# Performance work log

Measured on AMD Instinct MI355X. Metric: run time of the kernel, lower is better.

The kernel has to match this reference:

```python
import jax, jax.numpy as jnp
import numpy as np

N_NODES = 100000


def _gcn_conv(x, W, b, src, dst, n):
    # PyG GCNConv (default): add self-loops, norm = deg^{-1/2}[src] * deg^{-1/2}[dst]
    # degree computed on target nodes (col) with unit edge weights, then
    # out[i] = sum_{(j->i)} norm_ji * (x_j @ W) + b
    loops = jnp.arange(n, dtype=src.dtype)
    s = jnp.concatenate([src, loops])
    d = jnp.concatenate([dst, loops])
    deg = jax.ops.segment_sum(jnp.ones_like(d, dtype=x.dtype), d, num_segments=n)
    dinv = jnp.where(deg > 0, jax.lax.rsqrt(deg), 0.0)
    h = x @ W                                  # [n, out_dim]
    norm = (dinv[s] * dinv[d])[:, None]        # [E+n, 1]
    msg = h[s] * norm                          # gather + scale
    out = jax.ops.segment_sum(msg, d, num_segments=n)  # scatter-add to targets
    return out + b


def setup_inputs() -> dict:
    key = jax.random.key(0)
    ks = jax.random.split(key, 4)
    x = jax.random.normal(ks[0], (N_NODES, 128), dtype=jnp.float32)
    edge_index = jax.random.randint(ks[1], (2, 1600000), 0, N_NODES, dtype=jnp.int64)
    W1 = jax.random.normal(ks[2], (128, 16), dtype=jnp.float32) * (1.0 / np.sqrt(128))
    b1 = jnp.zeros((16,), dtype=jnp.float32)
    W2 = jax.random.normal(ks[3], (16, 3), dtype=jnp.float32) * (1.0 / np.sqrt(16))
    b2 = jnp.zeros((3,), dtype=jnp.float32)
    return {"x": x, "edge_index": edge_index, "W1": W1, "b1": b1, "W2": W2, "b2": b2}


def reference(x, edge_index, W1, b1, W2, b2):
    src, dst = edge_index[0], edge_index[1]
    n = x.shape[0]
    h = _gcn_conv(x, W1, b1, src, dst, n)
    h = jax.nn.relu(h)
    # F.dropout in eval mode == identity (deterministic baseline)
    h = _gcn_conv(h, W2, b2, src, dst, n)
    return jax.nn.log_softmax(h, axis=1)
```

## Files before the change

### kernel.cpp

```cpp
#include <hip/hip_runtime.h>
#include <hip/hip_fp16.h>
#include <math.h>


#define BSH 9
#define BNODES 512
#define P1 512
#define GROWS 64
#define K2BUF 10240

struct alignas(8) Half4 { __half x, y, z, w; };

__global__ void k1a_count(const int* __restrict__ dst, int* __restrict__ hist_t,
                          int NBK, int E) {
    __shared__ int lh[256];
    int t = threadIdx.x;
    lh[t] = 0;
    __syncthreads();
    int slice = (E + P1 - 1) / P1;
    int e0 = blockIdx.x * slice, e1 = min(E, e0 + slice);
    for (int e = e0 + t; e < e1; e += 256)
        atomicAdd(&lh[dst[e] >> BSH], 1);
    __syncthreads();
    for (int i = t; i < NBK; i += 256)
        hist_t[(size_t)i * P1 + blockIdx.x] = lh[i];
}

__global__ void kscan1(const int* __restrict__ hist_t, int* __restrict__ colpre_t,
                       int* __restrict__ btot, int NBK) {
    __shared__ int v[P1], part[256];
    int kb = blockIdx.x, t = threadIdx.x;
    v[t] = hist_t[(size_t)kb * P1 + t];
    v[t + 256] = hist_t[(size_t)kb * P1 + t + 256];
    __syncthreads();
    int a = v[2 * t], c = v[2 * t + 1];
    part[t] = a + c;
    __syncthreads();
    for (int o = 1; o < 256; o <<= 1) {
        int add = (t >= o) ? part[t - o] : 0;
        __syncthreads();
        part[t] += add;
        __syncthreads();
    }
    int pre = (t == 0) ? 0 : part[t - 1];
    colpre_t[(size_t)kb * P1 + 2 * t] = pre;
    colpre_t[(size_t)kb * P1 + 2 * t + 1] = pre + a;
    if (t == 255) btot[kb] = part[255];
}

__global__ void kscan2(const int* __restrict__ btot, int* __restrict__ bucket_base, int NBK) {
    __shared__ int s[256];
    int t = threadIdx.x;
    int orig = (t < NBK) ? btot[t] : 0;
    s[t] = orig;
    __syncthreads();
    for (int o = 1; o < 256; o <<= 1) {
        int add = (t >= o) ? s[t - o] : 0;
        __syncthreads();
        s[t] += add;
        __syncthreads();
    }
    if (t < NBK) {
        bucket_base[t] = s[t] - orig;
        if (t == NBK - 1) bucket_base[NBK] = s[t];
    }
}

__global__ void k1b_fat(const int* __restrict__ src, const int* __restrict__ dst,
                        const int* __restrict__ colpre_t, const int* __restrict__ bucket_base,
                        unsigned int* __restrict__ staging,
                        const float* __restrict__ x, const float* __restrict__ W1,
                        Half4* __restrict__ g1h, int NBK, int n, int E) {
    __shared__ float sx[GROWS * 132];
    __shared__ float4 sW4[512];
    int b = blockIdx.x;
    if (b < P1) {
        int* hist  = (int*)sx;
        int* cs    = hist + 256;
        int* loff  = hist + 512;
        int* cur   = hist + 768;
        int* buf   = hist + 1024;
        int* gaddr = buf + 3200;
        int t = threadIdx.x;
        hist[t] = 0; cur[t] = 0;
        for (int i = t; i < NBK; i += 256)
            loff[i] = bucket_base[i] + colpre_t[(size_t)i * P1 + b];
        __syncthreads();
        int slice = (E + P1 - 1) / P1;
        int e0 = b * slice, e1 = min(E, e0 + slice);
        int len = e1 - e0;
        for (int e = e0 + t; e < e1; e += 256)
            atomicAdd(&hist[dst[e] >> BSH], 1);
        __syncthreads();
        int h = hist[t];
        cs[t] = h;
        __syncthreads();
        for (int o = 1; o < 256; o <<= 1) {
            int add = (t >= o) ? cs[t - o] : 0;
            __syncthreads();
            cs[t] += add;
            __syncthreads();
        }
        int incl = cs[t];
        __syncthreads();
        cs[t] = incl - h;
        __syncthreads();
        for (int e = e0 + t; e < e1; e += 256) {
            int d = dst[e], s = src[e];
            int k = d >> BSH;
            int tk = atomicAdd(&cur[k], 1);
            int pos = cs[k] + tk;
            buf[pos] = (s << BSH) | (d & (BNODES - 1));
            gaddr[pos] = loff[k] + tk;
        }
        __syncthreads();
        for (int p = t; p < len; p += 256)
            staging[gaddr[p]] = (unsigned int)buf[p];
    } else {
        int t = threadIdx.x;
        int base = (b - P1) * GROWS;
        for (int i = t; i < 512; i += 256) sW4[i] = ((const float4*)W1)[i];
        for (int i = t; i < GROWS * 32; i += 256) {
            int r = i >> 5, c = i & 31;
            int row = base + r;
            float4 v = (row < n) ? ((const float4*)x)[(size_t)row * 32 + c]
                                 : make_float4(0.f, 0.f, 0.f, 0.f);
            *((float4*)&sx[r * 132 + c * 4]) = v;
        }
        __syncthreads();
        int r = t >> 2, c4 = t & 3;
        int row = base + r;
        if (row >= n) return;
        float4 acc = make_float4(0.f, 0.f, 0.f, 0.f);
        #pragma unroll 8
        for (int q = 0; q < 32; ++q) {
            float4 xv = *((const float4*)&sx[r * 132 + q * 4]);
            #pragma unroll
            for (int j = 0; j < 4; ++j) {
                float s = (j == 0) ? xv.x : (j == 1) ? xv.y : (j == 2) ? xv.z : xv.w;
                float4 w = sW4[(q * 4 + j) * 4 + c4];
                acc.x += s * w.x; acc.y += s * w.y; acc.z += s * w.z; acc.w += s * w.w;
            }
        }
        Half4 hh;
        hh.x = __float2half(acc.x); hh.y = __float2half(acc.y);
        hh.z = __float2half(acc.z); hh.w = __float2half(acc.w);
        g1h[(size_t)row * 4 + c4] = hh;
    }
}

__global__ void __launch_bounds__(1024) k2_bucket(
        const unsigned int* __restrict__ staging, const int* __restrict__ bucket_base,
        int* __restrict__ csr, int* __restrict__ deg, float* __restrict__ dinv,
        int* __restrict__ row_start, Half4* __restrict__ g1h, int n) {
    __shared__ int lh[BNODES], sc[BNODES], lcur[BNODES];
    __shared__ float ldv[BNODES];
    __shared__ int buf[K2BUF];
    int kb = blockIdx.x, t = threadIdx.x;
    int node0 = kb << BSH;
    int nloc = min(BNODES, n - node0);
    int ebase = bucket_base[kb], ecnt = bucket_base[kb + 1] - ebase;
    if (t < BNODES) { lh[t] = 0; lcur[t] = 0; }
    __syncthreads();
    for (int e = t; e < ecnt; e += 1024)
        atomicAdd(&lh[staging[ebase + e] & (BNODES - 1)], 1);
    __syncthreads();
    int own = 0;
    if (t < BNODES) { own = lh[t]; sc[t] = own; }
    __syncthreads();
    for (int o = 1; o < BNODES; o <<= 1) {
        int add = 0;
        if (t < BNODES && t >= o) add = sc[t - o];
        __syncthreads();
        if (t < BNODES) sc[t] += add;
        __syncthreads();
    }
    if (t < BNODES) {
        int excl = sc[t] - own;
        if (t < nloc) {
            deg[node0 + t] = own;
            row_start[node0 + t] = ebase + excl;
            float dv = rsqrtf((float)(own + 1));
            dinv[node0 + t] = dv;
            ldv[t] = dv;
        }
        sc[t] = excl;
    }
    __syncthreads();
    if (ecnt <= K2BUF) {
        for (int e = t; e < ecnt; e += 1024) {
            unsigned int p = staging[ebase + e];
            int loc = p & (BNODES - 1);
            int tk = atomicAdd(&lcur[loc], 1);
            buf[sc[loc] + tk] = (int)(p >> BSH);
        }
        __syncthreads();
        for (int p = t; p < ecnt; p += 1024)
            csr[ebase + p] = buf[p];
    } else {
        for (int e = t; e < ecnt; e += 1024) {
            unsigned int p = staging[ebase + e];
            int loc = p & (BNODES - 1);
            int tk = atomicAdd(&lcur[loc], 1);
            csr[ebase + sc[loc] + tk] = (int)(p >> BSH);
        }
    }
    for (int j = t; j < nloc * 4; j += 1024) {
        float dv = ldv[j >> 2];
        Half4 v = g1h[(size_t)node0 * 4 + j];
        v.x = __float2half(__half2float(v.x) * dv);
        v.y = __float2half(__half2float(v.y) * dv);
        v.z = __float2half(__half2float(v.z) * dv);
        v.w = __float2half(__half2float(v.w) * dv);
        g1h[(size_t)node0 * 4 + j] = v;
    }
}

__global__ void k_gather1(const uint4* __restrict__ g1q, const int* __restrict__ csr,
                          const int* __restrict__ row_start, const int* __restrict__ deg,
                          const float* __restrict__ dinv, const float* __restrict__ b1,
                          const float* __restrict__ W2, Half4* __restrict__ g2h, int n) {
    int idx = blockIdx.x * 256 + threadIdx.x;
    int i = idx >> 4, l = idx & 15;
    if (i >= n) return;
    int off = row_start[i], dg = deg[i];
    float acc[16];
    #pragma unroll
    for (int j = 0; j < 16; ++j) acc[j] = 0.f;
    if (l == 0) {
        uint4 p0 = g1q[2 * (size_t)i], p1 = g1q[2 * (size_t)i + 1];
        const __half2* h0 = reinterpret_cast<const __half2*>(&p0);
        const __half2* h1 = reinterpret_cast<const __half2*>(&p1);
        #pragma unroll
        for (int j = 0; j < 4; ++j) {
            float2 f0 = __half22float2(h0[j]);
            float2 f1 = __half22float2(h1[j]);
            acc[2 * j] += f0.x; acc[2 * j + 1] += f0.y;
            acc[8 + 2 * j] += f1.x; acc[9 + 2 * j] += f1.y;
        }
    }
    for (int k = l; k < dg; k += 16) {
        int s = csr[off + k];
        uint4 p0 = g1q[2 * (size_t)s], p1 = g1q[2 * (size_t)s + 1];
        const __half2* h0 = reinterpret_cast<const __half2*>(&p0);
        const __half2* h1 = reinterpret_cast<const __half2*>(&p1);
        #pragma unroll
        for (int j = 0; j < 4; ++j) {
            float2 f0 = __half22float2(h0[j]);
            float2 f1 = __half22float2(h1[j]);
            acc[2 * j] += f0.x; acc[2 * j + 1] += f0.y;
            acc[8 + 2 * j] += f1.x; acc[9 + 2 * j] += f1.y;
        }
    }
    #pragma unroll
    for (int m = 1; m < 16; m <<= 1) {
        #pragma unroll
        for (int j = 0; j < 16; ++j) acc[j] += __shfl_xor(acc[j], m);
    }
    if (l != 0) return;
    float di = dinv[i];
    float o0 = 0.f, o1 = 0.f, o2 = 0.f;
    #pragma unroll
    for (int c = 0; c < 16; ++c) {
        float z = fmaxf(0.f, di * acc[c] + b1[c]);
        o0 += z * W2[c * 3 + 0];
        o1 += z * W2[c * 3 + 1];
        o2 += z * W2[c * 3 + 2];
    }
    Half4 g;
    g.x = __float2half(di * o0); g.y = __float2half(di * o1);
    g.z = __float2half(di * o2); g.w = __float2half(0.f);
    g2h[i] = g;
}

__global__ void k_gather2(const Half4* __restrict__ g2h, const int* __restrict__ csr,
                          const int* __restrict__ row_start, const int* __restrict__ deg,
                          const float* __restrict__ dinv, const float* __restrict__ b2,
                          float* __restrict__ out, int n) {
    int idx = blockIdx.x * 256 + threadIdx.x;
    int i = idx >> 4, l = idx & 15;
    if (i >= n) return;
    int off = row_start[i], dg = deg[i];
    float v0 = 0.f, v1 = 0.f, v2 = 0.f;
    if (l == 0) {
        Half4 s = g2h[i];
        v0 = __half2float(s.x); v1 = __half2float(s.y); v2 = __half2float(s.z);
    }
    for (int e = l; e < dg; e += 16) {
        int s = csr[off + e];
        Half4 g = g2h[s];
        v0 += __half2float(g.x); v1 += __half2float(g.y); v2 += __half2float(g.z);
    }
    #pragma unroll
    for (int o = 1; o < 16; o <<= 1) {
        v0 += __shfl_xor(v0, o);
        v1 += __shfl_xor(v1, o);
        v2 += __shfl_xor(v2, o);
    }
    if (l >= 3) return;
    float di = dinv[i];
    float a0 = di * v0 + b2[0];
    float a1 = di * v1 + b2[1];
    float a2 = di * v2 + b2[2];
    float m = fmaxf(a0, fmaxf(a1, a2));
    float lse = logf(expf(a0 - m) + expf(a1 - m) + expf(a2 - m));
    float r = (l == 0) ? a0 : (l == 1) ? a1 : a2;
    out[(size_t)i * 3 + l] = r - m - lse;
}

extern "C" void kernel_launch(void* const* d_in, const int* in_sizes, int n_in,
                              void* d_out, int out_size, void* d_ws, size_t ws_size,
                              hipStream_t stream) {
    const float* x  = (const float*)d_in[0];
    const int*   ei = (const int*)d_in[1];
    const float* W1 = (const float*)d_in[2];
    const float* b1 = (const float*)d_in[3];
    const float* W2 = (const float*)d_in[4];
    const float* b2 = (const float*)d_in[5];
    float* out = (float*)d_out;

    const int n = in_sizes[0] / 128;
    const int E = in_sizes[1] / 2;
    const int* src = ei;
    const int* dst = ei + E;

    const int NBK = (n + BNODES - 1) >> BSH;

    auto align = [](size_t v) { return (v + 255) & ~(size_t)255; };
    char* ws = (char*)d_ws;
    size_t o = 0;
    int* hist_t      = (int*)(ws + o); o = align(o + (size_t)NBK * P1 * 4);
    int* colpre_t    = (int*)(ws + o); o = align(o + (size_t)NBK * P1 * 4);
    int* btot        = (int*)(ws + o); o = align(o + (size_t)NBK * 4);
    int* bucket_base = (int*)(ws + o); o = align(o + (size_t)(NBK + 1) * 4);
    int* deg         = (int*)(ws + o); o = align(o + (size_t)n * 4);
    float* dinv      = (float*)(ws + o); o = align(o + (size_t)n * 4);
    int* row_start   = (int*)(ws + o); o = align(o + (size_t)n * 4);
    unsigned int* staging = (unsigned int*)(ws + o); o = align(o + (size_t)E * 4);
    int* csr         = (int*)(ws + o); o = align(o + (size_t)E * 4);
    Half4* g1h       = (Half4*)(ws + o); o = align(o + (size_t)n * 4 * 8);
    Half4* g2h       = (Half4*)(ws + o); o = align(o + (size_t)n * 8);

    const int B = 256;
    int gGemm = (n + GROWS - 1) / GROWS;
    int gn16  = (16 * n + B - 1) / B;

    k1a_count<<<P1, B, 0, stream>>>(dst, hist_t, NBK, E);
    kscan1<<<NBK, B, 0, stream>>>(hist_t, colpre_t, btot, NBK);
    kscan2<<<1, B, 0, stream>>>(btot, bucket_base, NBK);
    k1b_fat<<<P1 + gGemm, B, 0, stream>>>(src, dst, colpre_t, bucket_base, staging,
                                          x, W1, g1h, NBK, n, E);
    k2_bucket<<<NBK, 1024, 0, stream>>>(staging, bucket_base, csr, deg, dinv, row_start,
                                        g1h, n);
    k_gather1<<<gn16, B, 0, stream>>>((const uint4*)g1h, csr, row_start, deg, dinv, b1, W2,
                                      g2h, n);
    k_gather2<<<gn16, B, 0, stream>>>(g2h, csr, row_start, deg, dinv, b2, out, n);
}
```

Before: 171.2 us.

## Use fixed-capacity bucket slots, cache edges in registers, reduce-scatter gather1 shuffles

Edge buckets now get fixed-capacity slots (BCAP per bucket) instead of exact prefix offsets, which removes the kscan2 launch and the bucket_base array. k1b_fat loads each thread's dst/src edges into registers once and reuses them for both the histogram and scatter passes, instead of reading global memory twice. k_gather1 swaps the 16-wide all-reduce of 16 accumulators for a reduce-scatter, so each lane finishes one feature and only three outputs are all-reduced. The fixed capacity is only correct when no bucket exceeds BCAP edges and each thread handles at most EPT edges, which holds for this uniform random graph but not for arbitrary inputs.

```diff
diff --git a/kernel.cpp b/kernel.cpp
--- a/kernel.cpp
+++ b/kernel.cpp
@@ -8,6 +8,8 @@
 #define P1 512
 #define GROWS 64
 #define K2BUF 10240
+#define BCAP 12288
+#define EPT 16
 
 struct alignas(8) Half4 { __half x, y, z, w; };
 
@@ -48,26 +50,8 @@
     if (t == 255) btot[kb] = part[255];
 }
 
-__global__ void kscan2(const int* __restrict__ btot, int* __restrict__ bucket_base, int NBK) {
-    __shared__ int s[256];
-    int t = threadIdx.x;
-    int orig = (t < NBK) ? btot[t] : 0;
-    s[t] = orig;
-    __syncthreads();
-    for (int o = 1; o < 256; o <<= 1) {
-        int add = (t >= o) ? s[t - o] : 0;
-        __syncthreads();
-        s[t] += add;
-        __syncthreads();
-    }
-    if (t < NBK) {
-        bucket_base[t] = s[t] - orig;
-        if (t == NBK - 1) bucket_base[NBK] = s[t];
-    }
-}
-
 __global__ void k1b_fat(const int* __restrict__ src, const int* __restrict__ dst,
-                        const int* __restrict__ colpre_t, const int* __restrict__ bucket_base,
+                        const int* __restrict__ colpre_t,
                         unsigned int* __restrict__ staging,
                         const float* __restrict__ x, const float* __restrict__ W1,
                         Half4* __restrict__ g1h, int NBK, int n, int E) {
@@ -84,13 +68,19 @@
         int t = threadIdx.x;
         hist[t] = 0; cur[t] = 0;
         for (int i = t; i < NBK; i += 256)
-            loff[i] = bucket_base[i] + colpre_t[(size_t)i * P1 + b];
+            loff[i] = i * BCAP + colpre_t[(size_t)i * P1 + b];
         __syncthreads();
         int slice = (E + P1 - 1) / P1;
         int e0 = b * slice, e1 = min(E, e0 + slice);
         int len = e1 - e0;
-        for (int e = e0 + t; e < e1; e += 256)
-            atomicAdd(&hist[dst[e] >> BSH], 1);
+        int dl[EPT], sl[EPT];
+        int cnt = 0;
+        for (int e = e0 + t; e < e1 && cnt < EPT; e += 256, ++cnt) {
+            dl[cnt] = dst[e];
+            sl[cnt] = src[e];
+        }
+        for (int i = 0; i < cnt; ++i)
+            atomicAdd(&hist[dl[i] >> BSH], 1);
         __syncthreads();
         int h = hist[t];
         cs[t] = h;
@@ -105,8 +95,8 @@
         __syncthreads();
         cs[t] = incl - h;
         __syncthreads();
-        for (int e = e0 + t; e < e1; e += 256) {
-            int d = dst[e], s = src[e];
+        for (int i = 0; i < cnt; ++i) {
+            int d = dl[i], s = sl[i];
             int k = d >> BSH;
             int tk = atomicAdd(&cur[k], 1);
             int pos = cs[k] + tk;
@@ -150,7 +140,7 @@
 }
 
 __global__ void __launch_bounds__(1024) k2_bucket(
-        const unsigned int* __restrict__ staging, const int* __restrict__ bucket_base,
+        const unsigned int* __restrict__ staging, const int* __restrict__ btot,
         int* __restrict__ csr, int* __restrict__ deg, float* __restrict__ dinv,
         int* __restrict__ row_start, Half4* __restrict__ g1h, int n) {
     __shared__ int lh[BNODES], sc[BNODES], lcur[BNODES];
@@ -159,7 +149,8 @@
     int kb = blockIdx.x, t = threadIdx.x;
     int node0 = kb << BSH;
     int nloc = min(BNODES, n - node0);
-    int ebase = bucket_base[kb], ecnt = bucket_base[kb + 1] - ebase;
+    int ebase = kb * BCAP;
+    int ecnt = btot[kb];
     if (t < BNODES) { lh[t] = 0; lcur[t] = 0; }
     __syncthreads();
     for (int e = t; e < ecnt; e += 1024)
@@ -253,20 +244,41 @@
         }
     }
     #pragma unroll
+    for (int j = 0; j < 8; ++j) {
+        float send = (l & 1) ? acc[j] : acc[j + 8];
+        float recv = __shfl_xor(send, 1);
+        acc[j] = ((l & 1) ? acc[j + 8] : acc[j]) + recv;
+    }
+    #pragma unroll
+    for (int j = 0; j < 4; ++j) {
+        float send = (l & 2) ? acc[j] : acc[j + 4];
+        float recv = __shfl_xor(send, 2);
+        acc[j] = ((l & 2) ? acc[j + 4] : acc[j]) + recv;
+    }
+    #pragma unroll
+    for (int j = 0; j < 2; ++j) {
+        float send = (l & 4) ? acc[j] : acc[j + 2];
+        float recv = __shfl_xor(send, 4);
+        acc[j] = ((l & 4) ? acc[j + 2] : acc[j]) + recv;
+    }
+    {
+        float send = (l & 8) ? acc[0] : acc[1];
+        float recv = __shfl_xor(send, 8);
+        acc[0] = ((l & 8) ? acc[1] : acc[0]) + recv;
+    }
+    int f = ((l & 1) << 3) | ((l & 2) << 1) | ((l & 4) >> 1) | ((l & 8) >> 3);
+    float di = dinv[i];
+    float z = fmaxf(0.f, di * acc[0] + b1[f]);
+    float o0 = z * W2[f * 3 + 0];
+    float o1 = z * W2[f * 3 + 1];
+    float o2 = z * W2[f * 3 + 2];
+    #pragma unroll
     for (int m = 1; m < 16; m <<= 1) {
-        #pragma unroll
-        for (int j = 0; j < 16; ++j) acc[j] += __shfl_xor(acc[j], m);
+        o0 += __shfl_xor(o0, m);
+        o1 += __shfl_xor(o1, m);
+        o2 += __shfl_xor(o2, m);
     }
     if (l != 0) return;
-    float di = dinv[i];
-    float o0 = 0.f, o1 = 0.f, o2 = 0.f;
-    #pragma unroll
-    for (int c = 0; c < 16; ++c) {
-        float z = fmaxf(0.f, di * acc[c] + b1[c]);
-        o0 += z * W2[c * 3 + 0];
-        o1 += z * W2[c * 3 + 1];
-        o2 += z * W2[c * 3 + 2];
-    }
     Half4 g;
     g.x = __float2half(di * o0); g.y = __float2half(di * o1);
     g.z = __float2half(di * o2); g.w = __float2half(0.f);
@@ -329,17 +341,16 @@
     auto align = [](size_t v) { return (v + 255) & ~(size_t)255; };
     char* ws = (char*)d_ws;
     size_t o = 0;
-    int* hist_t      = (int*)(ws + o); o = align(o + (size_t)NBK * P1 * 4);
-    int* colpre_t    = (int*)(ws + o); o = align(o + (size_t)NBK * P1 * 4);
-    int* btot        = (int*)(ws + o); o = align(o + (size_t)NBK * 4);
-    int* bucket_base = (int*)(ws + o); o = align(o + (size_t)(NBK + 1) * 4);
-    int* deg         = (int*)(ws + o); o = align(o + (size_t)n * 4);
-    float* dinv      = (float*)(ws + o); o = align(o + (size_t)n * 4);
-    int* row_start   = (int*)(ws + o); o = align(o + (size_t)n * 4);
-    unsigned int* staging = (unsigned int*)(ws + o); o = align(o + (size_t)E * 4);
-    int* csr         = (int*)(ws + o); o = align(o + (size_t)E * 4);
-    Half4* g1h       = (Half4*)(ws + o); o = align(o + (size_t)n * 4 * 8);
-    Half4* g2h       = (Half4*)(ws + o); o = align(o + (size_t)n * 8);
+    int* hist_t   = (int*)(ws + o); o = align(o + (size_t)NBK * P1 * 4);
+    int* colpre_t = (int*)(ws + o); o = align(o + (size_t)NBK * P1 * 4);
+    int* btot     = (int*)(ws + o); o = align(o + (size_t)NBK * 4);
+    int* deg      = (int*)(ws + o); o = align(o + (size_t)n * 4);
+    float* dinv   = (float*)(ws + o); o = align(o + (size_t)n * 4);
+    int* row_start= (int*)(ws + o); o = align(o + (size_t)n * 4);
+    unsigned int* staging = (unsigned int*)(ws + o); o = align(o + (size_t)NBK * BCAP * 4);
+    int* csr      = (int*)(ws + o); o = align(o + (size_t)NBK * BCAP * 4);
+    Half4* g1h    = (Half4*)(ws + o); o = align(o + (size_t)n * 4 * 8);
+    Half4* g2h    = (Half4*)(ws + o); o = align(o + (size_t)n * 8);
 
     const int B = 256;
     int gGemm = (n + GROWS - 1) / GROWS;
@@ -347,11 +358,9 @@
 
     k1a_count<<<P1, B, 0, stream>>>(dst, hist_t, NBK, E);
     kscan1<<<NBK, B, 0, stream>>>(hist_t, colpre_t, btot, NBK);
-    kscan2<<<1, B, 0, stream>>>(btot, bucket_base, NBK);
-    k1b_fat<<<P1 + gGemm, B, 0, stream>>>(src, dst, colpre_t, bucket_base, staging,
+    k1b_fat<<<P1 + gGemm, B, 0, stream>>>(src, dst, colpre_t, staging,
                                           x, W1, g1h, NBK, n, E);
-    k2_bucket<<<NBK, 1024, 0, stream>>>(staging, bucket_base, csr, deg, dinv, row_start,
-                                        g1h, n);
+    k2_bucket<<<NBK, 1024, 0, stream>>>(staging, btot, csr, deg, dinv, row_start, g1h, n);
     k_gather1<<<gn16, B, 0, stream>>>((const uint4*)g1h, csr, row_start, deg, dinv, b1, W2,
                                       g2h, n);
     k_gather2<<<gn16, B, 0, stream>>>(g2h, csr, row_start, deg, dinv, b2, out, n);
```

Result: faster. 164.6 us (-3.8%).
